# Optimization experiments

Measured on AMD Instinct MI355X. Metric: run time of the kernel, lower is better.

The kernel has to match this reference:

```python
import jax, jax.numpy as jnp
import numpy as np
from jax import lax

# --- RPN config (eval / TEST path) ---
ASPECT = (0.5, 1.0, 2.0)
SCALE = (8.0, 16.0, 32.0)
STRIDE = 16
N_ANCHORS = len(ASPECT) * len(SCALE)  # 9
PRE_NMS = 6000
POST_NMS = 300
NMS_THRESH = 0.7
MIN_SIZE = 16.0
NEG = jnp.float32(-1e9)


def conv2d(x, w, b, pad):
    y = lax.conv_general_dilated(x, w, (1, 1), [(pad, pad), (pad, pad)],
                                 dimension_numbers=('NCHW', 'OIHW', 'NCHW'))
    return y + b[None, :, None, None]


def make_anchors(h, w):
    asp = jnp.array(ASPECT, jnp.float32)
    sc = jnp.array(SCALE, jnp.float32)
    size = float(STRIDE * STRIDE)
    ws = (jnp.sqrt(size / asp)[:, None] * sc[None, :]).reshape(-1)  # (A,)
    hs = (jnp.sqrt(size * asp)[:, None] * sc[None, :]).reshape(-1)
    c = (STRIDE - 1) / 2.0
    base = jnp.stack([c - 0.5 * (ws - 1), c - 0.5 * (hs - 1),
                      c + 0.5 * (ws - 1), c + 0.5 * (hs - 1)], axis=-1)  # (A,4)
    sx = jnp.arange(w, dtype=jnp.float32) * STRIDE
    sy = jnp.arange(h, dtype=jnp.float32) * STRIDE
    shift_x, shift_y = jnp.meshgrid(sx, sy)  # (h,w)
    shifts = jnp.stack([shift_x, shift_y, shift_x, shift_y], axis=-1)  # (h,w,4)
    return (shifts[:, :, None, :] + base[None, None]).reshape(-1, 4)  # (h*w*A,4)


def decode_boxes(anchors, deltas):
    wa = anchors[..., 2] - anchors[..., 0] + 1.0
    ha = anchors[..., 3] - anchors[..., 1] + 1.0
    cxa = anchors[..., 0] + 0.5 * wa
    cya = anchors[..., 1] + 0.5 * ha
    cx = deltas[..., 0] * wa + cxa
    cy = deltas[..., 1] * ha + cya
    pw = jnp.exp(deltas[..., 2]) * wa
    ph = jnp.exp(deltas[..., 3]) * ha
    return jnp.stack([cx - 0.5 * pw, cy - 0.5 * ph,
                      cx + 0.5 * pw, cy + 0.5 * ph], axis=-1)


def iou_one_many(box, boxes):
    x1 = jnp.maximum(box[0], boxes[:, 0])
    y1 = jnp.maximum(box[1], boxes[:, 1])
    x2 = jnp.minimum(box[2], boxes[:, 2])
    y2 = jnp.minimum(box[3], boxes[:, 3])
    inter = jnp.maximum(0.0, x2 - x1 + 1.0) * jnp.maximum(0.0, y2 - y1 + 1.0)
    a0 = (box[2] - box[0] + 1.0) * (box[3] - box[1] + 1.0)
    a1 = (boxes[:, 2] - boxes[:, 0] + 1.0) * (boxes[:, 3] - boxes[:, 1] + 1.0)
    return inter / (a0 + a1 - inter)


def nms_keep(boxes, scores):
    # boxes: (PRE,4) sorted by score desc; returns POST_NMS kept indices
    n = boxes.shape[0]

    def body(i, carry):
        valid, keep = carry
        s = jnp.where(valid, scores, NEG)
        j = jnp.argmax(s).astype(jnp.int32)
        keep = keep.at[i].set(j)
        iou = iou_one_many(boxes[j], boxes)
        valid = valid & (iou <= NMS_THRESH)
        valid = valid.at[j].set(False)
        return valid, keep

    _, keep = lax.fori_loop(0, POST_NMS, body,
                            (jnp.ones(n, bool), jnp.zeros(POST_NMS, jnp.int32)))
    return keep


def rpn_forward(input, im_info, w_feat, b_feat, w_cls, b_cls, w_reg, b_reg):
    feat = jax.nn.relu(conv2d(input, w_feat, b_feat, 1))  # (B,512,h,w)
    cls = conv2d(feat, w_cls, b_cls, 0)                    # (B,2A,h,w)
    B, _, h, w = cls.shape
    prob = jax.nn.softmax(cls.reshape(B, N_ANCHORS, 2, h, w), axis=2)
    fg = prob[:, :, 1]                                     # (B,A,h,w)
    scores = fg.transpose(0, 2, 3, 1).reshape(B, h * w * N_ANCHORS)
    reg = conv2d(feat, w_reg, b_reg, 0)                    # (B,4A,h,w)
    deltas = reg.transpose(0, 2, 3, 1).reshape(B, h * w * N_ANCHORS, 4)

    anchors = make_anchors(h, w)                           # (K,4)
    boxes = decode_boxes(anchors[None], deltas)            # (B,K,4)

    # clip to image
    im_h = im_info[:, 0][:, None]
    im_w = im_info[:, 1][:, None]
    x1 = jnp.clip(boxes[..., 0], 0.0, im_w - 1.0)
    y1 = jnp.clip(boxes[..., 1], 0.0, im_h - 1.0)
    x2 = jnp.clip(boxes[..., 2], 0.0, im_w - 1.0)
    y2 = jnp.clip(boxes[..., 3], 0.0, im_h - 1.0)
    boxes = jnp.stack([x1, y1, x2, y2], axis=-1)

    # min-size filter (mask scores instead of dropping rows)
    ms = MIN_SIZE * im_info[:, 2][:, None]
    ok = ((x2 - x1 + 1.0) >= ms) & ((y2 - y1 + 1.0) >= ms)
    scores = jnp.where(ok, scores, NEG)

    top_scores, order = lax.top_k(scores, PRE_NMS)         # (B,PRE)
    boxes_sorted = jnp.take_along_axis(boxes, order[..., None], axis=1)
    keep = jax.vmap(nms_keep)(boxes_sorted, top_scores)    # (B,POST)
    rois_boxes = jnp.take_along_axis(boxes_sorted, keep[..., None], axis=1)
    bidx = jnp.broadcast_to(jnp.arange(B, dtype=boxes.dtype)[:, None, None],
                            (B, POST_NMS, 1))
    return jnp.concatenate([bidx, rois_boxes], axis=-1)    # (B,POST,5)


def setup_inputs() -> dict:
    key = jax.random.key(0)
    ks = jax.random.split(key, 8)
    B, C, H, W = 8, 512, 64, 64
    inp = {
        'input': jax.random.normal(ks[0], (B, C, H, W), jnp.float32),
        'gt_box': jnp.zeros((B, 20, 5), jnp.float32),
        'im_info': jnp.tile(jnp.array([[1024.0, 1024.0, 1.0]], jnp.float32), (B, 1)),
        'w_feat': jax.random.normal(ks[1], (512, 512, 3, 3), jnp.float32) * 0.01,
        'b_feat': jnp.zeros((512,), jnp.float32),
        'w_cls': jax.random.normal(ks[2], (2 * N_ANCHORS, 512, 1, 1), jnp.float32) * 0.01,
        'b_cls': jnp.zeros((2 * N_ANCHORS,), jnp.float32),
        'w_reg': jax.random.normal(ks[3], (4 * N_ANCHORS, 512, 1, 1), jnp.float32) * 0.01,
        'b_reg': jnp.zeros((4 * N_ANCHORS,), jnp.float32),
    }
    return inp


def reference(input, gt_box, im_info, w_feat, b_feat, w_cls, b_cls, w_reg, b_reg):
    # eval-mode RPN: module returns (0, 0, rois); we return rois
    return rpn_forward(input, im_info, w_feat, b_feat, w_cls, b_cls, w_reg, b_reg)
```

## Files before the change

### kernel.cpp

```cpp
#include <hip/hip_runtime.h>
#include <hip/hip_bf16.h>
#include <stdint.h>

#define HW      64
#define CIN     512
#define KOUT    512
#define BATCH   8
#define NANCH   9
#define NBOX    (HW*HW*NANCH)
#define PRE_NMS 6000
#define POST_NMS 300
#define SORT_N  8192

__global__ __launch_bounds__(256)
void transpose_w(const float* __restrict__ w, float* __restrict__ wt) {
    __shared__ float t[32][33];
    const int jt = blockIdx.x * 32, kt = blockIdx.y * 32;
    const int c  = threadIdx.x & 31, r8 = threadIdx.x >> 5;
#pragma unroll
    for (int p = 0; p < 4; ++p) {
        int kl = r8 + p * 8;
        t[kl][c] = w[(size_t)(kt + kl) * 4608 + jt + c];
    }
    __syncthreads();
#pragma unroll
    for (int p = 0; p < 4; ++p) {
        int jl = r8 + p * 8;
        wt[(size_t)(jt + jl) * 512 + kt + c] = t[c][jl];
    }
}

__global__ __launch_bounds__(256, 2)
void conv3x3_relu(const float* __restrict__ in, const float* __restrict__ wt,
                  const float* __restrict__ bias, float* __restrict__ feat) {
    __shared__ float s_in[2][4 * 6 * 68 + 4];
    __shared__ float s_w[2][36][64];

    const int tid = threadIdx.x;
    const int k0  = blockIdx.x * 64;
    const int y0  = blockIdx.y * 4;
    const int b   = blockIdx.z;
    const int kg  = tid & 7;
    const int pos = tid >> 3;
    const int tx  = pos & 15;
    const int ty  = pos >> 4;
    const int x0  = tx * 4;

    int in_lds[2]; int in_goff[2]; bool in_act[2], in_ok[2];
#pragma unroll
    for (int s = 0; s < 2; ++s) {
        int q   = tid + 256 * s;
        bool a  = (q < 384);
        int qq  = a ? q : 0;
        int ci  = qq / 96, rem = qq % 96;
        int r   = rem >> 4, c4 = rem & 15;
        int gy  = y0 - 1 + r;
        in_act[s] = a;
        in_ok[s]  = a && ((unsigned)gy < 64u);
        int gyc   = gy < 0 ? 0 : (gy > 63 ? 63 : gy);
        in_lds[s] = 4 + (ci * 6 + r) * 68 + 4 * c4;
        in_goff[s] = ((b * 512 + ci) * 64 + gyc) * 64 + 4 * c4;
    }
    int w_lds[3]; int w_goff[3]; bool w_act[3];
#pragma unroll
    for (int s = 0; s < 3; ++s) {
        int q  = tid + 256 * s;
        bool a = (q < 576);
        int qq = a ? q : 0;
        int jl = qq / 16, k4 = qq % 16;
        w_act[s]  = a;
        w_lds[s]  = jl * 64 + 4 * k4;
        w_goff[s] = jl * 512 + k0 + 4 * k4;
    }

    for (int i = tid; i < 2 * (4 * 6 * 68 + 4); i += 256) ((float*)s_in)[i] = 0.0f;
    __syncthreads();

    float4 pin[2], pw[3];
    const float4 z4 = make_float4(0.f, 0.f, 0.f, 0.f);
    auto prefetch = [&](int cc4) {
#pragma unroll
        for (int s = 0; s < 2; ++s)
            pin[s] = in_ok[s] ? *(const float4*)&in[in_goff[s] + cc4 * 16384] : z4;
#pragma unroll
        for (int s = 0; s < 3; ++s)
            if (w_act[s]) pw[s] = *(const float4*)&wt[(size_t)cc4 * 18432 + w_goff[s]];
    };
    prefetch(0);

    float acc[2][8][4];
#pragma unroll
    for (int r = 0; r < 2; ++r)
#pragma unroll
        for (int k = 0; k < 8; ++k)
#pragma unroll
            for (int c = 0; c < 4; ++c) acc[r][k][c] = 0.0f;

    for (int cc4 = 0; cc4 < 128; ++cc4) {
        float* SIN = &s_in[cc4 & 1][0];
        float* SW  = &s_w[cc4 & 1][0][0];

#pragma unroll
        for (int s = 0; s < 2; ++s)
            if (in_act[s]) *(float4*)&SIN[in_lds[s]] = pin[s];
#pragma unroll
        for (int s = 0; s < 3; ++s)
            if (w_act[s]) *(float4*)&SW[w_lds[s]] = pw[s];
        __syncthreads();
        if (cc4 < 127) prefetch(cc4 + 1);

#pragma unroll
        for (int ci = 0; ci < 4; ++ci) {
#pragma unroll
            for (int dy = 0; dy < 3; ++dy) {
                float iv[2][6];
#pragma unroll
                for (int rr = 0; rr < 2; ++rr) {
                    int rw = ty * 2 + rr + dy;
                    const float* rp = &SIN[4 + (ci * 6 + rw) * 68];
                    float4 va = *(const float4*)&rp[x0];
                    iv[rr][0] = rp[x0 - 1];
                    iv[rr][1] = va.x; iv[rr][2] = va.y;
                    iv[rr][3] = va.z; iv[rr][4] = va.w;
                    iv[rr][5] = rp[x0 + 4];
                }
#pragma unroll
                for (int dx = 0; dx < 3; ++dx) {
                    const float* wp = &SW[(ci * 9 + dy * 3 + dx) * 64 + kg * 8];
                    float4 w0v = *(const float4*)wp;
                    float4 w1v = *(const float4*)(wp + 4);
                    float wv[8] = {w0v.x, w0v.y, w0v.z, w0v.w,
                                   w1v.x, w1v.y, w1v.z, w1v.w};
#pragma unroll
                    for (int rr = 0; rr < 2; ++rr)
#pragma unroll
                        for (int k = 0; k < 8; ++k)
#pragma unroll
                            for (int c = 0; c < 4; ++c)
                                acc[rr][k][c] = fmaf(iv[rr][dx + c], wv[k], acc[rr][k][c]);
                }
            }
        }
    }
#pragma unroll
    for (int k = 0; k < 8; ++k) {
        float bv = bias[k0 + kg * 8 + k];
#pragma unroll
        for (int rr = 0; rr < 2; ++rr) {
            int y = y0 + ty * 2 + rr;
            float4 o;
            o.x = fmaxf(acc[rr][k][0] + bv, 0.0f);
            o.y = fmaxf(acc[rr][k][1] + bv, 0.0f);
            o.z = fmaxf(acc[rr][k][2] + bv, 0.0f);
            o.w = fmaxf(acc[rr][k][3] + bv, 0.0f);
            *(float4*)&feat[(((size_t)b * KOUT + k0 + kg * 8 + k) * HW + y) * HW + x0] = o;
        }
    }
}

__global__ __launch_bounds__(128, 2)
void heads(const float* __restrict__ feat,
           const float* __restrict__ wcls, const float* __restrict__ bcls,
           const float* __restrict__ wreg, const float* __restrict__ breg,
           const float* __restrict__ iminfo,
           unsigned long long* __restrict__ keys, float4* __restrict__ pbox) {
    __shared__ float s_w[128 * 56];

    const int tid = threadIdx.x;
    const int pix = blockIdx.x * 128 + tid;
    const int b   = pix >> 12;
    const int rem = pix & 4095;
    const int y   = rem >> 6;
    const int x   = rem & 63;

    float acc[54];
#pragma unroll
    for (int j = 0; j < 54; ++j) acc[j] = 0.0f;

    for (int cc = 0; cc < 512; cc += 128) {
        __syncthreads();
        for (int i = tid; i < 128 * 56; i += 128) {
            int cl = i / 56; int j = i % 56;
            float v = 0.0f;
            if (j < 18)      v = wcls[(size_t)j * 512 + cc + cl];
            else if (j < 54) v = wreg[(size_t)(j - 18) * 512 + cc + cl];
            s_w[i] = v;
        }
        __syncthreads();
#pragma unroll 4
        for (int c2 = 0; c2 < 128; ++c2) {
            float f = feat[(((size_t)b * 512 + cc + c2) * 64 + y) * 64 + x];
            const float* wr = &s_w[c2 * 56];
#pragma unroll
            for (int j4 = 0; j4 < 13; ++j4) {
                float4 w4 = *(const float4*)&wr[4 * j4];
                acc[4 * j4 + 0] = fmaf(f, w4.x, acc[4 * j4 + 0]);
                acc[4 * j4 + 1] = fmaf(f, w4.y, acc[4 * j4 + 1]);
                acc[4 * j4 + 2] = fmaf(f, w4.z, acc[4 * j4 + 2]);
                acc[4 * j4 + 3] = fmaf(f, w4.w, acc[4 * j4 + 3]);
            }
            float4 wt4 = *(const float4*)&wr[52];
            acc[52] = fmaf(f, wt4.x, acc[52]);
            acc[53] = fmaf(f, wt4.y, acc[53]);
        }
    }

    const float im_h = iminfo[b * 3 + 0];
    const float im_w = iminfo[b * 3 + 1];
    const float ms   = 16.0f * iminfo[b * 3 + 2];
    const float ASP[3] = {0.5f, 1.0f, 2.0f};
    const float SCL[3] = {8.0f, 16.0f, 32.0f};

#pragma unroll
    for (int a = 0; a < 9; ++a) {
        float c0 = acc[2 * a]     + bcls[2 * a];
        float c1 = acc[2 * a + 1] + bcls[2 * a + 1];
        float m  = fmaxf(c0, c1);
        float e0 = expf(c0 - m), e1 = expf(c1 - m);
        float fg = e1 / (e0 + e1);

        float d0 = acc[18 + 4 * a + 0] + breg[4 * a + 0];
        float d1 = acc[18 + 4 * a + 1] + breg[4 * a + 1];
        float d2 = acc[18 + 4 * a + 2] + breg[4 * a + 2];
        float d3 = acc[18 + 4 * a + 3] + breg[4 * a + 3];

        int ai = a / 3, si = a % 3;
        float wsz = sqrtf(256.0f / ASP[ai]) * SCL[si];
        float hsz = sqrtf(256.0f * ASP[ai]) * SCL[si];
        float sx = (float)x * 16.0f, sy = (float)y * 16.0f;
        float x1a = sx + (7.5f - 0.5f * (wsz - 1.0f));
        float y1a = sy + (7.5f - 0.5f * (hsz - 1.0f));
        float x2a = sx + (7.5f + 0.5f * (wsz - 1.0f));
        float y2a = sy + (7.5f + 0.5f * (hsz - 1.0f));

        float wa = x2a - x1a + 1.0f, ha = y2a - y1a + 1.0f;
        float cxa = x1a + 0.5f * wa, cya = y1a + 0.5f * ha;
        float cx = d0 * wa + cxa, cy = d1 * ha + cya;
        float pw = expf(d2) * wa, ph = expf(d3) * ha;
        float bx1 = cx - 0.5f * pw, by1 = cy - 0.5f * ph;
        float bx2 = cx + 0.5f * pw, by2 = cy + 0.5f * ph;

        bx1 = fminf(fmaxf(bx1, 0.0f), im_w - 1.0f);
        by1 = fminf(fmaxf(by1, 0.0f), im_h - 1.0f);
        bx2 = fminf(fmaxf(bx2, 0.0f), im_w - 1.0f);
        by2 = fminf(fmaxf(by2, 0.0f), im_h - 1.0f);

        bool ok = (bx2 - bx1 + 1.0f >= ms) && (by2 - by1 + 1.0f >= ms);
        float s = ok ? fg : -1e9f;

        unsigned u = __float_as_uint(s);
        u = (u & 0x80000000u) ? ~u : (u | 0x80000000u);
        int idx = (y * 64 + x) * 9 + a;
        keys[(size_t)b * NBOX + idx] =
            ((unsigned long long)u << 32) | (unsigned)(~(unsigned)idx);
        pbox[(size_t)b * NBOX + idx] = make_float4(bx1, by1, bx2, by2);
    }
}

__global__ __launch_bounds__(1024)
void select_sort(const unsigned long long* __restrict__ keys,
                 const float4* __restrict__ pbox,
                 float4* __restrict__ sorted) {
    __shared__ unsigned long long sbuf[SORT_N];
    __shared__ unsigned hist[16][256];
    __shared__ unsigned sh_prefix, sh_remaining, sh_counter;

    const int tid = threadIdx.x;
    const int b   = blockIdx.x;
    const int wv  = tid >> 6;
    const unsigned long long* kb = keys + (size_t)b * NBOX;

    if (tid == 0) { sh_prefix = 0u; sh_remaining = PRE_NMS; sh_counter = 0u; }

    for (int p = 3; p >= 0; --p) {
        for (int i = tid; i < 16 * 256; i += 1024) ((unsigned*)hist)[i] = 0u;
        __syncthreads();
        unsigned prefix = sh_prefix;
        unsigned pmask  = (p == 3) ? 0u : (0xFFFFFFFFu << (8 * (p + 1)));
        for (int i = tid; i < NBOX; i += 1024) {
            unsigned u = (unsigned)(kb[i] >> 32);
            if ((u & pmask) == prefix)
                atomicAdd(&hist[wv][(u >> (8 * p)) & 255], 1u);
        }
        __syncthreads();
        if (tid < 256) {
            unsigned s = 0;
#pragma unroll
            for (int w2 = 0; w2 < 16; ++w2) s += hist[w2][tid];
            hist[0][tid] = s;
        }
        __syncthreads();
        if (tid == 0) {
            unsigned rem = sh_remaining;
            int v = 255;
            for (; v > 0; --v) {
                unsigned c = hist[0][v];
                if (rem <= c) break;
                rem -= c;
            }
            sh_prefix    = prefix | ((unsigned)v << (8 * p));
            sh_remaining = rem;
        }
        __syncthreads();
    }
    const unsigned thr = sh_prefix;

    for (int i = tid; i < NBOX; i += 1024) {
        unsigned long long k = kb[i];
        bool act = ((unsigned)(k >> 32) >= thr);
        unsigned long long bal = __ballot(act);
        if (act) {
            int lane   = tid & 63;
            int leader = __ffsll(bal) - 1;
            unsigned base = 0;
            if (lane == leader) base = atomicAdd(&sh_counter, (unsigned)__popcll(bal));
            base = __shfl(base, leader);
            unsigned off = (unsigned)__popcll(bal & ((1ull << lane) - 1ull));
            unsigned pos2 = base + off;
            if (pos2 < SORT_N) sbuf[pos2] = k;
        }
    }
    __syncthreads();
    unsigned n = sh_counter; if (n > SORT_N) n = SORT_N;
    for (int i = (int)n + tid; i < SORT_N; i += 1024) sbuf[i] = 0ull;
    __syncthreads();

    for (int k = 2; k <= SORT_N; k <<= 1) {
        for (int j = k >> 1; j > 0; j >>= 1) {
            for (int t = tid; t < SORT_N / 2; t += 1024) {
                int i  = ((t & ~(j - 1)) << 1) | (t & (j - 1));
                int ix = i | j;
                bool up = ((i & k) == 0);
                unsigned long long a = sbuf[i], c = sbuf[ix];
                bool sw = up ? (a < c) : (a > c);
                if (sw) { sbuf[i] = c; sbuf[ix] = a; }
            }
            __syncthreads();
        }
    }

    for (int i = tid; i < PRE_NMS; i += 1024) {
        unsigned idx = ~((unsigned)sbuf[i]);
        sorted[(size_t)b * PRE_NMS + i] = pbox[(size_t)b * NBOX + idx];
    }
}

__global__ __launch_bounds__(512, 2)
void nms(const float4* __restrict__ sorted, float* __restrict__ out) {
    __shared__ unsigned long long vmask[94];
    __shared__ int sh_j;

    const int tid = threadIdx.x;
    const int b   = blockIdx.x;
    const float4* sb = sorted + (size_t)b * PRE_NMS;

    float4 bx[12]; float ar[12];
#pragma unroll
    for (int s = 0; s < 12; ++s) {
        int i = tid + 512 * s;
        if (i < PRE_NMS) {
            float4 v = sb[i];
            bx[s] = v;
            ar[s] = (v.z - v.x + 1.0f) * (v.w - v.y + 1.0f);
        } else {
            bx[s] = make_float4(0.f, 0.f, 0.f, 0.f);
            ar[s] = 1.0f;
        }
    }
    if (tid < 94) vmask[tid] = (tid < 93) ? ~0ull : ((1ull << 48) - 1ull);
    __syncthreads();

    for (int it = 0; it < POST_NMS; ++it) {
        if (tid < 64) {
            unsigned long long w0 = vmask[tid];
            unsigned long long w1 = (tid < 30) ? vmask[tid + 64] : 0ull;
            int cand = w0 ? (tid * 64 + __ffsll(w0) - 1)
                          : (w1 ? ((tid + 64) * 64 + __ffsll(w1) - 1) : 0x7FFFFFFF);
#pragma unroll
            for (int off = 32; off > 0; off >>= 1) {
                int o = __shfl_xor(cand, off);
                cand = (o < cand) ? o : cand;
            }
            if (tid == 0) sh_j = (cand == 0x7FFFFFFF) ? 0 : cand;
        }
        __syncthreads();
        int j = sh_j;
        float4 jb = sb[j];
        if (tid == 0) {
            float* o = out + ((size_t)b * POST_NMS + it) * 5;
            o[0] = (float)b; o[1] = jb.x; o[2] = jb.y; o[3] = jb.z; o[4] = jb.w;
        }
        float ja = (jb.z - jb.x + 1.0f) * (jb.w - jb.y + 1.0f);
#pragma unroll
        for (int s = 0; s < 12; ++s) {
            int i = tid + 512 * s;
            if (i < PRE_NMS && ((vmask[i >> 6] >> (i & 63)) & 1ull)) {
                float xx1 = fmaxf(jb.x, bx[s].x);
                float yy1 = fmaxf(jb.y, bx[s].y);
                float xx2 = fminf(jb.z, bx[s].z);
                float yy2 = fminf(jb.w, bx[s].w);
                float inter = fmaxf(0.0f, xx2 - xx1 + 1.0f) *
                              fmaxf(0.0f, yy2 - yy1 + 1.0f);
                float iou = inter / (ja + ar[s] - inter);
                if (iou > 0.7f)
                    atomicAnd(&vmask[i >> 6], ~(1ull << (i & 63)));
            }
        }
        __syncthreads();
    }
}

extern "C" void kernel_launch(void* const* d_in, const int* in_sizes, int n_in,
                              void* d_out, int out_size, void* d_ws, size_t ws_size,
                              hipStream_t stream) {
    (void)in_sizes; (void)n_in; (void)out_size; (void)ws_size;
    const float* input  = (const float*)d_in[0];
    const float* iminfo = (const float*)d_in[2];
    const float* wfeat  = (const float*)d_in[3];
    const float* bfeat  = (const float*)d_in[4];
    const float* wcls   = (const float*)d_in[5];
    const float* bcls   = (const float*)d_in[6];
    const float* wreg   = (const float*)d_in[7];
    const float* breg   = (const float*)d_in[8];
    float* out = (float*)d_out;

    char* ws = (char*)d_ws;
    float*               feat   = (float*)ws;
    float*               wt     = (float*)(ws + 67108864);
    unsigned long long*  keys   = (unsigned long long*)(ws + 67108864);
    float4*              pbox   = (float4*)(ws + 67108864 + 2359296);
    float4*              sorted = (float4*)(ws + 67108864 + 2359296 + 4718592);

    transpose_w<<<dim3(144, 16), 256, 0, stream>>>(wfeat, wt);
    conv3x3_relu<<<dim3(8, 16, 8), 256, 0, stream>>>(input, wt, bfeat, feat);
    heads<<<dim3(256), 128, 0, stream>>>(feat, wcls, bcls, wreg, breg, iminfo, keys, pbox);
    select_sort<<<dim3(8), 1024, 0, stream>>>(keys, pbox, sorted);
    nms<<<dim3(8), 512, 0, stream>>>(sorted, out);
}
```

Baseline: 3.377 ms.

## Restructure 3x3 conv tiling to one row per block with wave-uniform weight loads

The conv kernel now gives each block a single output row, with one pixel per thread and 16 output channels per wave. Weights are read directly from global memory at a wave-uniform address (readfirstlane) instead of being staged in LDS, so they can go through scalar or broadcast loads. Input rows are staged eight channels at a time. Arithmetic intensity per thread falls sharply: each input value is reused across only 16 channels rather than 8x8 outputs. Input halo reloading also grows, from 6 rows per 4 outputs to 3 rows per 1 output, which risks a slower kernel.

```diff
diff --git a/kernel.cpp b/kernel.cpp
--- a/kernel.cpp
+++ b/kernel.cpp
@@ -30,21 +30,18 @@
     }
 }
 
-__global__ __launch_bounds__(256, 2)
+__global__ __launch_bounds__(256)
 void conv3x3_relu(const float* __restrict__ in, const float* __restrict__ wt,
                   const float* __restrict__ bias, float* __restrict__ feat) {
-    __shared__ float s_in[2][4 * 6 * 68 + 4];
-    __shared__ float s_w[2][36][64];
+    __shared__ float s_in[2][8 * 3 * 68 + 4];
 
     const int tid = threadIdx.x;
     const int k0  = blockIdx.x * 64;
-    const int y0  = blockIdx.y * 4;
+    const int y   = blockIdx.y;
     const int b   = blockIdx.z;
-    const int kg  = tid & 7;
-    const int pos = tid >> 3;
-    const int tx  = pos & 15;
-    const int ty  = pos >> 4;
-    const int x0  = tx * 4;
+    const int x   = tid & 63;
+    const int kw  = __builtin_amdgcn_readfirstlane(tid >> 6);
+    const int kb  = k0 + kw * 16;
 
     int in_lds[2]; int in_goff[2]; bool in_act[2], in_ok[2];
 #pragma unroll
@@ -52,109 +49,71 @@
         int q   = tid + 256 * s;
         bool a  = (q < 384);
         int qq  = a ? q : 0;
-        int ci  = qq / 96, rem = qq % 96;
+        int ci  = qq / 48, rem = qq % 48;
         int r   = rem >> 4, c4 = rem & 15;
-        int gy  = y0 - 1 + r;
+        int gy  = y - 1 + r;
         in_act[s] = a;
         in_ok[s]  = a && ((unsigned)gy < 64u);
         int gyc   = gy < 0 ? 0 : (gy > 63 ? 63 : gy);
-        in_lds[s] = 4 + (ci * 6 + r) * 68 + 4 * c4;
+        in_lds[s] = 4 + (ci * 3 + r) * 68 + 4 * c4;
         in_goff[s] = ((b * 512 + ci) * 64 + gyc) * 64 + 4 * c4;
     }
-    int w_lds[3]; int w_goff[3]; bool w_act[3];
-#pragma unroll
-    for (int s = 0; s < 3; ++s) {
-        int q  = tid + 256 * s;
-        bool a = (q < 576);
-        int qq = a ? q : 0;
-        int jl = qq / 16, k4 = qq % 16;
-        w_act[s]  = a;
-        w_lds[s]  = jl * 64 + 4 * k4;
-        w_goff[s] = jl * 512 + k0 + 4 * k4;
-    }
-
-    for (int i = tid; i < 2 * (4 * 6 * 68 + 4); i += 256) ((float*)s_in)[i] = 0.0f;
-    __syncthreads();
-
-    float4 pin[2], pw[3];
+
+    for (int i = tid; i < 2 * (8 * 3 * 68 + 4); i += 256) ((float*)s_in)[i] = 0.0f;
+    __syncthreads();
+
+    float4 pin[2];
     const float4 z4 = make_float4(0.f, 0.f, 0.f, 0.f);
-    auto prefetch = [&](int cc4) {
+    auto prefetch = [&](int cc8) {
 #pragma unroll
         for (int s = 0; s < 2; ++s)
-            pin[s] = in_ok[s] ? *(const float4*)&in[in_goff[s] + cc4 * 16384] : z4;
-#pragma unroll
-        for (int s = 0; s < 3; ++s)
-            if (w_act[s]) pw[s] = *(const float4*)&wt[(size_t)cc4 * 18432 + w_goff[s]];
+            pin[s] = in_ok[s] ? *(const float4*)&in[in_goff[s] + cc8 * 32768] : z4;
     };
     prefetch(0);
 
-    float acc[2][8][4];
-#pragma unroll
-    for (int r = 0; r < 2; ++r)
-#pragma unroll
-        for (int k = 0; k < 8; ++k)
-#pragma unroll
-            for (int c = 0; c < 4; ++c) acc[r][k][c] = 0.0f;
-
-    for (int cc4 = 0; cc4 < 128; ++cc4) {
-        float* SIN = &s_in[cc4 & 1][0];
-        float* SW  = &s_w[cc4 & 1][0][0];
+    float acc[16];
+#pragma unroll
+    for (int k = 0; k < 16; ++k) acc[k] = 0.0f;
+
+    for (int cc8 = 0; cc8 < 64; ++cc8) {
+        float* SIN = &s_in[cc8 & 1][0];
 
 #pragma unroll
         for (int s = 0; s < 2; ++s)
             if (in_act[s]) *(float4*)&SIN[in_lds[s]] = pin[s];
-#pragma unroll
-        for (int s = 0; s < 3; ++s)
-            if (w_act[s]) *(float4*)&SW[w_lds[s]] = pw[s];
-        __syncthreads();
-        if (cc4 < 127) prefetch(cc4 + 1);
-
-#pragma unroll
-        for (int ci = 0; ci < 4; ++ci) {
+        __syncthreads();
+        if (cc8 < 63) prefetch(cc8 + 1);
+
+#pragma unroll
+        for (int ci = 0; ci < 8; ++ci) {
 #pragma unroll
             for (int dy = 0; dy < 3; ++dy) {
-                float iv[2][6];
-#pragma unroll
-                for (int rr = 0; rr < 2; ++rr) {
-                    int rw = ty * 2 + rr + dy;
-                    const float* rp = &SIN[4 + (ci * 6 + rw) * 68];
-                    float4 va = *(const float4*)&rp[x0];
-                    iv[rr][0] = rp[x0 - 1];
-                    iv[rr][1] = va.x; iv[rr][2] = va.y;
-                    iv[rr][3] = va.z; iv[rr][4] = va.w;
-                    iv[rr][5] = rp[x0 + 4];
+                const float* rp = &SIN[4 + (ci * 3 + dy) * 68];
+                float ivv[3];
+                ivv[0] = rp[x - 1];
+                ivv[1] = rp[x];
+                ivv[2] = rp[x + 1];
+#pragma unroll
+                for (int dx = 0; dx < 3; ++dx) {
+                    const float* wp = &wt[(size_t)((cc8 * 8 + ci) * 9 + dy * 3 + dx) * 512 + kb];
+                    float4 wA = *(const float4*)(wp);
+                    float4 wB = *(const float4*)(wp + 4);
+                    float4 wC = *(const float4*)(wp + 8);
+                    float4 wD = *(const float4*)(wp + 12);
+                    float wv[16] = {wA.x, wA.y, wA.z, wA.w, wB.x, wB.y, wB.z, wB.w,
+                                    wC.x, wC.y, wC.z, wC.w, wD.x, wD.y, wD.z, wD.w};
+                    float f = ivv[dx];
+#pragma unroll
+                    for (int k = 0; k < 16; ++k)
+                        acc[k] = fmaf(f, wv[k], acc[k]);
                 }
-#pragma unroll
-                for (int dx = 0; dx < 3; ++dx) {
-                    const float* wp = &SW[(ci * 9 + dy * 3 + dx) * 64 + kg * 8];
-                    float4 w0v = *(const float4*)wp;
-                    float4 w1v = *(const float4*)(wp + 4);
-                    float wv[8] = {w0v.x, w0v.y, w0v.z, w0v.w,
-                                   w1v.x, w1v.y, w1v.z, w1v.w};
-#pragma unroll
-                    for (int rr = 0; rr < 2; ++rr)
-#pragma unroll
-                        for (int k = 0; k < 8; ++k)
-#pragma unroll
-                            for (int c = 0; c < 4; ++c)
-                                acc[rr][k][c] = fmaf(iv[rr][dx + c], wv[k], acc[rr][k][c]);
-                }
-            }
-        }
-    }
-#pragma unroll
-    for (int k = 0; k < 8; ++k) {
-        float bv = bias[k0 + kg * 8 + k];
-#pragma unroll
-        for (int rr = 0; rr < 2; ++rr) {
-            int y = y0 + ty * 2 + rr;
-            float4 o;
-            o.x = fmaxf(acc[rr][k][0] + bv, 0.0f);
-            o.y = fmaxf(acc[rr][k][1] + bv, 0.0f);
-            o.z = fmaxf(acc[rr][k][2] + bv, 0.0f);
-            o.w = fmaxf(acc[rr][k][3] + bv, 0.0f);
-            *(float4*)&feat[(((size_t)b * KOUT + k0 + kg * 8 + k) * HW + y) * HW + x0] = o;
-        }
+            }
+        }
+    }
+#pragma unroll
+    for (int k = 0; k < 16; ++k) {
+        float v = fmaxf(acc[k] + bias[kb + k], 0.0f);
+        feat[(((size_t)b * KOUT + kb + k) * HW + y) * HW + x] = v;
     }
 }
 
@@ -432,7 +391,7 @@
     float4*              sorted = (float4*)(ws + 67108864 + 2359296 + 4718592);
 
     transpose_w<<<dim3(144, 16), 256, 0, stream>>>(wfeat, wt);
-    conv3x3_relu<<<dim3(8, 16, 8), 256, 0, stream>>>(input, wt, bfeat, feat);
+    conv3x3_relu<<<dim3(8, 64, 8), 256, 0, stream>>>(input, wt, bfeat, feat);
     heads<<<dim3(256), 128, 0, stream>>>(feat, wcls, bcls, wreg, breg, iminfo, keys, pbox);
     select_sort<<<dim3(8), 1024, 0, stream>>>(keys, pbox, sorted);
     nms<<<dim3(8), 512, 0, stream>>>(sorted, out);
```

Result: no change. 3.364 ms (-0.4%).
